# Kernel optimization log

Hardware: AMD Instinct MI355X
Metric: run time of the kernel (lower is better)

Reference implementation:

```python
import jax, jax.numpy as jnp
import numpy as np


def setup_inputs() -> dict:
    key = jax.random.key(0)
    H, W, C, N = 200, 200, 256, 2000
    img = jax.random.normal(key, (1, H, W, C), dtype=jnp.float32)
    rng = np.random.RandomState(0)
    x = rng.randint(0, W - 50, size=N)
    y = rng.randint(0, H - 50, size=N)
    w = rng.randint(8, 50, size=N)
    h = rng.randint(8, 50, size=N)
    rois = jnp.asarray(np.stack([x, y, w, h], axis=-1)[None].astype(np.float32))
    return {"img": img, "rois": rois, "pool_size": 7}


def _roi_bilinear(feat, roi, ps):
    # feat: (H, W, C); roi: int32 (x, y, w, h) -> (ps, ps, C)
    # Mirrors TF1 tf.image.resize_images bilinear, align_corners=False:
    # src coordinate inside the crop = out_idx * (crop_size / ps).
    H, W = feat.shape[0], feat.shape[1]
    x, y, w, h = roi[0], roi[1], roi[2], roi[3]
    sy = h.astype(jnp.float32) / ps
    sx = w.astype(jnp.float32) / ps
    src_y = jnp.arange(ps, dtype=jnp.float32) * sy
    src_x = jnp.arange(ps, dtype=jnp.float32) * sx
    y0 = jnp.floor(src_y).astype(jnp.int32)
    x0 = jnp.floor(src_x).astype(jnp.int32)
    wy = src_y - y0.astype(jnp.float32)
    wx = src_x - x0.astype(jnp.float32)
    # clamp inside the crop, then translate to global image coords (and clamp for safety)
    gy0 = jnp.clip(y + jnp.clip(y0, 0, h - 1), 0, H - 1)
    gy1 = jnp.clip(y + jnp.clip(y0 + 1, 0, h - 1), 0, H - 1)
    gx0 = jnp.clip(x + jnp.clip(x0, 0, w - 1), 0, W - 1)
    gx1 = jnp.clip(x + jnp.clip(x0 + 1, 0, w - 1), 0, W - 1)
    v00 = feat[gy0[:, None], gx0[None, :]]  # (ps, ps, C)
    v01 = feat[gy0[:, None], gx1[None, :]]
    v10 = feat[gy1[:, None], gx0[None, :]]
    v11 = feat[gy1[:, None], gx1[None, :]]
    wy = wy[:, None, None]
    wx = wx[None, :, None]
    top = v00 * (1.0 - wx) + v01 * wx
    bot = v10 * (1.0 - wx) + v11 * wx
    return top * (1.0 - wy) + bot * wy


def reference(img, rois, pool_size):
    feat = img[0]                          # (H, W, C)
    roi_int = rois[0].astype(jnp.int32)    # (N, 4) -- cast as in the 'tf' branch
    pooled = jax.vmap(lambda r: _roi_bilinear(feat, r, pool_size))(roi_int)
    return pooled[None]                    # (1, N, ps, ps, C)
```

## Files before the change

kernel.cpp:

```cpp
#include <hip/hip_runtime.h>


typedef float vfloat4 __attribute__((ext_vector_type(4)));

template <int PS>
__global__ __launch_bounds__(PS * 64) void RoIPool_rows_kernel(
    const float* __restrict__ feat,
    const float* __restrict__ rois,
    float*       __restrict__ out,
    int H, int W)
{
    constexpr int C4 = 64;
    const int roi  = blockIdx.x;
    const int py   = threadIdx.x >> 6;
    const int lane = threadIdx.x & 63;

    const float4 r = reinterpret_cast<const float4*>(rois)[roi];
    const int x = (int)r.x;
    const int y = (int)r.y;
    const int w = (int)r.z;
    const int h = (int)r.w;

    const float sy = (float)h / (float)PS;
    const float sx = (float)w / (float)PS;

    const float src_y = (float)py * sy;
    const int   y0    = (int)floorf(src_y);
    const float wy    = src_y - (float)y0;
    const float omwy  = 1.0f - wy;
    const int gy0 = min(max(y + min(max(y0,     0), h - 1), 0), H - 1);
    const int gy1 = min(max(y + min(max(y0 + 1, 0), h - 1), 0), H - 1);

    const float4* __restrict__ f4 = reinterpret_cast<const float4*>(feat);

    const int rb0 = gy0 * W * C4 + lane;
    const int rb1 = gy1 * W * C4 + lane;

    float4 v00[PS], v01[PS], v10[PS], v11[PS];
    float  wxa[PS];

#pragma unroll
    for (int px = 0; px < PS; ++px) {
        const float src_x = (float)px * sx;
        const int   x0    = (int)floorf(src_x);
        wxa[px] = src_x - (float)x0;
        const int gx0 = min(max(x + min(max(x0,     0), w - 1), 0), W - 1);
        const int gx1 = min(max(x + min(max(x0 + 1, 0), w - 1), 0), W - 1);
        v00[px] = f4[rb0 + gx0 * C4];
        v01[px] = f4[rb0 + gx1 * C4];
        v10[px] = f4[rb1 + gx0 * C4];
        v11[px] = f4[rb1 + gx1 * C4];
    }

    vfloat4* __restrict__ o4 = reinterpret_cast<vfloat4*>(out);
    const int ob = (roi * (PS * PS) + py * PS) * C4 + lane;

#pragma unroll
    for (int px = 0; px < PS; ++px) {
        const float wx   = wxa[px];
        const float omwx = 1.0f - wx;
        vfloat4 o;
        o.x = (v00[px].x * omwx + v01[px].x * wx) * omwy + (v10[px].x * omwx + v11[px].x * wx) * wy;
        o.y = (v00[px].y * omwx + v01[px].y * wx) * omwy + (v10[px].y * omwx + v11[px].y * wx) * wy;
        o.z = (v00[px].z * omwx + v01[px].z * wx) * omwy + (v10[px].z * omwx + v11[px].z * wx) * wy;
        o.w = (v00[px].w * omwx + v01[px].w * wx) * omwy + (v10[px].w * omwx + v11[px].w * wx) * wy;
        __builtin_nontemporal_store(o, o4 + ob + px * C4);
    }
}


__global__ __launch_bounds__(256) void RoIPool_53575422050620_kernel(
    const float* __restrict__ feat,
    const float* __restrict__ rois,
    const int*   __restrict__ psp,
    float*       __restrict__ out,
    int n_cells, int H, int W, int C)
{
    const int ps   = psp[0];
    const int cell = blockIdx.x * 4 + (threadIdx.x >> 6);
    if (cell >= n_cells) return;
    const int lane = threadIdx.x & 63;

    const int pp  = ps * ps;
    const int roi = cell / pp;
    const int rem = cell - roi * pp;
    const int py  = rem / ps;
    const int px  = rem - py * ps;

    const float4 r = reinterpret_cast<const float4*>(rois)[roi];
    const int x = (int)r.x;
    const int y = (int)r.y;
    const int w = (int)r.z;
    const int h = (int)r.w;

    const float sy    = (float)h / (float)ps;
    const float sx    = (float)w / (float)ps;
    const float src_y = (float)py * sy;
    const float src_x = (float)px * sx;
    const int y0 = (int)floorf(src_y);
    const int x0 = (int)floorf(src_x);
    const float wy = src_y - (float)y0;
    const float wx = src_x - (float)x0;

    const int gy0 = min(max(y + min(max(y0,     0), h - 1), 0), H - 1);
    const int gy1 = min(max(y + min(max(y0 + 1, 0), h - 1), 0), H - 1);
    const int gx0 = min(max(x + min(max(x0,     0), w - 1), 0), W - 1);
    const int gx1 = min(max(x + min(max(x0 + 1, 0), w - 1), 0), W - 1);

    const int C4 = C >> 2;
    const float4* __restrict__ f4 = reinterpret_cast<const float4*>(feat);
    float4* __restrict__ o4 = reinterpret_cast<float4*>(out);

    const size_t b00 = (size_t)(gy0 * W + gx0) * C4;
    const size_t b01 = (size_t)(gy0 * W + gx1) * C4;
    const size_t b10 = (size_t)(gy1 * W + gx0) * C4;
    const size_t b11 = (size_t)(gy1 * W + gx1) * C4;
    const size_t ob  = (size_t)cell * C4;

    const float omwx = 1.0f - wx;
    const float omwy = 1.0f - wy;

    for (int cv = lane; cv < C4; cv += 64) {
        const float4 v00 = f4[b00 + cv];
        const float4 v01 = f4[b01 + cv];
        const float4 v10 = f4[b10 + cv];
        const float4 v11 = f4[b11 + cv];
        float4 o;
        o.x = (v00.x * omwx + v01.x * wx) * omwy + (v10.x * omwx + v11.x * wx) * wy;
        o.y = (v00.y * omwx + v01.y * wx) * omwy + (v10.y * omwx + v11.y * wx) * wy;
        o.z = (v00.z * omwx + v01.z * wx) * omwy + (v10.z * omwx + v11.z * wx) * wy;
        o.w = (v00.w * omwx + v01.w * wx) * omwy + (v10.w * omwx + v11.w * wx) * wy;
        o4[ob + cv] = o;
    }
}

extern "C" void kernel_launch(void* const* d_in, const int* in_sizes, int n_in,
                              void* d_out, int out_size, void* d_ws, size_t ws_size,
                              hipStream_t stream) {
    const float* img  = (const float*)d_in[0];
    const float* rois = (const float*)d_in[1];
    const int*   psp  = (const int*)d_in[2];
    float*       out  = (float*)d_out;

    const int H = 200, W = 200, C = 256;
    const int n_cells = out_size / C;
    const int N  = in_sizes[1] / 4;
    const int pp = (N > 0) ? (n_cells / N) : 0;
    int ps = 1;
    while (ps * ps < pp) ++ps;

    if (N > 0 && pp == 49 && ps * ps == pp && ps * ps * N == n_cells && C == 256) {
        RoIPool_rows_kernel<7><<<N, 7 * 64, 0, stream>>>(img, rois, out, H, W);
    } else {
        const int blocks = (n_cells + 3) / 4;
        RoIPool_53575422050620_kernel<<<blocks, 256, 0, stream>>>(
            img, rois, psp, out, n_cells, H, W, C);
    }
}
```

Baseline: 169.1 us.

## Sort RoIs by Morton order and map spatial neighbours to same XCD

Adds a single-block bitonic sort kernel that orders RoIs by the Morton code of their centres and writes a permutation to the workspace. The main kernel then remaps block indices so consecutive sorted RoIs land on the same XCD (block id mod 8), aiming to improve L2 reuse of overlapping feature rows. This adds an extra serial kernel launch with many barriers, and it only applies when N is a multiple of 8 and at most 2048.

```diff
diff --git a/kernel.cpp b/kernel.cpp
--- a/kernel.cpp
+++ b/kernel.cpp
@@ -2,16 +2,72 @@
 
 
 typedef float vfloat4 __attribute__((ext_vector_type(4)));
+
+
+__global__ __launch_bounds__(256) void RoIPool_sort_kernel(
+    const float* __restrict__ rois, int N, unsigned* __restrict__ perm)
+{
+    constexpr int n = 2048;
+    __shared__ unsigned keys[n];
+    const int t = threadIdx.x;
+
+    for (int i = t; i < n; i += 256) {
+        unsigned v = 0xFFFFFFFFu;
+        if (i < N) {
+            const float4 r = reinterpret_cast<const float4*>(rois)[i];
+            int cx = (int)r.x + ((int)r.z >> 1);
+            int cy = (int)r.y + ((int)r.w >> 1);
+            cx = min(max(cx, 0), 255);
+            cy = min(max(cy, 0), 255);
+            unsigned mx = (unsigned)cx, my = (unsigned)cy;
+            mx = (mx | (mx << 4)) & 0x0F0Fu;
+            mx = (mx | (mx << 2)) & 0x3333u;
+            mx = (mx | (mx << 1)) & 0x5555u;
+            my = (my | (my << 4)) & 0x0F0Fu;
+            my = (my | (my << 2)) & 0x3333u;
+            my = (my | (my << 1)) & 0x5555u;
+            const unsigned key = mx | (my << 1);
+            v = (key << 11) | (unsigned)i;
+        }
+        keys[i] = v;
+    }
+    __syncthreads();
+
+    for (int k = 2; k <= n; k <<= 1) {
+        for (int j = k >> 1; j > 0; j >>= 1) {
+            for (int i = t; i < n; i += 256) {
+                const int ixj = i ^ j;
+                if (ixj > i) {
+                    const unsigned a = keys[i], b = keys[ixj];
+                    const bool up = ((i & k) == 0);
+                    if ((a > b) == up) { keys[i] = b; keys[ixj] = a; }
+                }
+            }
+            __syncthreads();
+        }
+    }
+
+    for (int i = t; i < N; i += 256) perm[i] = keys[i] & 0x7FFu;
+}
+
 
 template <int PS>
 __global__ __launch_bounds__(PS * 64) void RoIPool_rows_kernel(
     const float* __restrict__ feat,
     const float* __restrict__ rois,
+    const unsigned* __restrict__ perm,
     float*       __restrict__ out,
     int H, int W)
 {
     constexpr int C4 = 64;
-    const int roi  = blockIdx.x;
+    int roi;
+    if (perm) {
+        const int per_xcd = gridDim.x >> 3;
+        const int s = (blockIdx.x & 7) * per_xcd + (blockIdx.x >> 3);
+        roi = (int)perm[s];
+    } else {
+        roi = blockIdx.x;
+    }
     const int py   = threadIdx.x >> 6;
     const int lane = threadIdx.x & 63;
 
@@ -150,7 +206,12 @@
     while (ps * ps < pp) ++ps;
 
     if (N > 0 && pp == 49 && ps * ps == pp && ps * ps * N == n_cells && C == 256) {
-        RoIPool_rows_kernel<7><<<N, 7 * 64, 0, stream>>>(img, rois, out, H, W);
+        unsigned* perm = nullptr;
+        if (N <= 2048 && (N & 7) == 0 && ws_size >= (size_t)N * sizeof(unsigned)) {
+            perm = (unsigned*)d_ws;
+            RoIPool_sort_kernel<<<1, 256, 0, stream>>>(rois, N, perm);
+        }
+        RoIPool_rows_kernel<7><<<N, 7 * 64, 0, stream>>>(img, rois, perm, out, H, W);
     } else {
         const int blocks = (n_cells + 3) / 4;
         RoIPool_53575422050620_kernel<<<blocks, 256, 0, stream>>>(
```

Measured after the change: 227.7 us. 34.7% more time.

## Sort RoIs into spatial Morton bins and map bins to XCDs for L2 locality

Applied to the files above, without the earlier changes.

Adds a single-block pre-pass that buckets RoIs by Morton-ordered 16x16 spatial bins of their centre and writes a permutation to the workspace. The main kernel then reads its RoI through that permutation, remapping block indices so each XCD gets a contiguous run of spatially nearby RoIs. The aim is to raise L2 reuse of feature rows on each XCD's separate L2. The cost is an extra kernel launch with a serial single-block counting sort, plus an indirection load per block.

```diff
diff --git a/kernel.cpp b/kernel.cpp
--- a/kernel.cpp
+++ b/kernel.cpp
@@ -2,16 +2,75 @@
 
 
 typedef float vfloat4 __attribute__((ext_vector_type(4)));
+
+
+__global__ __launch_bounds__(1024) void RoIPool_bin_kernel(
+    const float* __restrict__ rois, int N, unsigned* __restrict__ perm)
+{
+    __shared__ unsigned cnt[256];
+    __shared__ unsigned scan[256];
+    const int t = threadIdx.x;
+
+    if (t < 256) cnt[t] = 0;
+    __syncthreads();
+
+    unsigned mybin[2];
+    int      myroi[2];
+    int      nmine = 0;
+    for (int i = t; i < N; i += 1024) {
+        const float4 r = reinterpret_cast<const float4*>(rois)[i];
+        const int cx = (int)r.x + ((int)r.z >> 1);
+        const int cy = (int)r.y + ((int)r.w >> 1);
+        unsigned bx = (unsigned)min(max(cx >> 4, 0), 15);
+        unsigned by = (unsigned)min(max(cy >> 4, 0), 15);
+        bx = (bx | (bx << 2)) & 0x33u;  bx = (bx | (bx << 1)) & 0x55u;
+        by = (by | (by << 2)) & 0x33u;  by = (by | (by << 1)) & 0x55u;
+        const unsigned bin = bx | (by << 1);
+        mybin[nmine] = bin;
+        myroi[nmine] = i;
+        ++nmine;
+        atomicAdd(&cnt[bin], 1u);
+    }
+    __syncthreads();
+
+    if (t < 256) scan[t] = cnt[t];
+    __syncthreads();
+    for (int off = 1; off < 256; off <<= 1) {
+        unsigned v = 0;
+        if (t < 256 && t >= off) v = scan[t - off];
+        __syncthreads();
+        if (t < 256) scan[t] += v;
+        __syncthreads();
+    }
+
+    if (t < 256) cnt[t] = 0;
+    __syncthreads();
+    for (int k = 0; k < nmine; ++k) {
+        const unsigned bin  = mybin[k];
+        const unsigned excl = (bin == 0) ? 0u : scan[bin - 1];
+        const unsigned pos  = excl + atomicAdd(&cnt[bin], 1u);
+        perm[pos] = (unsigned)myroi[k];
+    }
+}
+
 
 template <int PS>
 __global__ __launch_bounds__(PS * 64) void RoIPool_rows_kernel(
     const float* __restrict__ feat,
     const float* __restrict__ rois,
+    const unsigned* __restrict__ perm,
     float*       __restrict__ out,
     int H, int W)
 {
     constexpr int C4 = 64;
-    const int roi  = blockIdx.x;
+    int roi;
+    if (perm) {
+        const int per_xcd = gridDim.x >> 3;
+        const int s = (blockIdx.x & 7) * per_xcd + (blockIdx.x >> 3);
+        roi = (int)perm[s];
+    } else {
+        roi = blockIdx.x;
+    }
     const int py   = threadIdx.x >> 6;
     const int lane = threadIdx.x & 63;
 
@@ -150,7 +209,12 @@
     while (ps * ps < pp) ++ps;
 
     if (N > 0 && pp == 49 && ps * ps == pp && ps * ps * N == n_cells && C == 256) {
-        RoIPool_rows_kernel<7><<<N, 7 * 64, 0, stream>>>(img, rois, out, H, W);
+        unsigned* perm = nullptr;
+        if (N <= 2048 && (N & 7) == 0 && ws_size >= (size_t)N * sizeof(unsigned)) {
+            perm = (unsigned*)d_ws;
+            RoIPool_bin_kernel<<<1, 1024, 0, stream>>>(rois, N, perm);
+        }
+        RoIPool_rows_kernel<7><<<N, 7 * 64, 0, stream>>>(img, rois, perm, out, H, W);
     } else {
         const int blocks = (n_cells + 3) / 4;
         RoIPool_53575422050620_kernel<<<blocks, 256, 0, stream>>>(
```

Result: no change. 169.0 us (-0.1%).
